# Kernel tuning notes

Hardware: AMD Instinct MI355X
Metric: run time of the kernel (lower is better)

The kernel has to match this reference:

```python
import jax, jax.numpy as jnp
import numpy as np

B, C, H, W = 8, 32, 256, 256


def setup_inputs() -> dict:
    key = jax.random.key(0)
    ks = jax.random.split(key, 9)
    x = jax.random.normal(ks[0], (B, C, H, W), dtype=jnp.float32)
    # depthwise 1x1 conv (groups=C) == per-channel scalar weight + bias
    def wb(kw, kb):
        w = jax.random.normal(kw, (C,), dtype=jnp.float32) * (1.0 / jnp.sqrt(1.0))
        b = jax.random.normal(kb, (C,), dtype=jnp.float32) * 0.1
        return w, b
    w_up, b_up = wb(ks[1], ks[2])
    w_right, b_right = wb(ks[3], ks[4])
    w_down, b_down = wb(ks[5], ks[6])
    w_left, b_left = wb(ks[7], ks[8])
    return {"x": x, "w_up": w_up, "b_up": b_up, "w_right": w_right,
            "b_right": b_right, "w_down": w_down, "b_down": b_down,
            "w_left": w_left, "b_left": b_left}


def _dir_scan(x_seq, w, b):
    """x_seq: [L, B, C, K]. h[0]=x[0]; h[t+1]=relu(w_c*h[t]+b_c+x[t+1])."""
    wb_ = w[None, :, None]
    bb_ = b[None, :, None]

    def step(h, xt):
        hn = jax.nn.relu(h * wb_ + bb_ + xt)
        return hn, hn

    _, ys = jax.lax.scan(step, x_seq[0], x_seq[1:])
    return jnp.concatenate([x_seq[:1], ys], axis=0)


def reference(x, w_up, b_up, w_right, b_right, w_down, b_down, w_left, b_left):
    xh = jnp.moveaxis(x, 2, 0)  # [H, B, C, W] for row scans
    xw = jnp.moveaxis(x, 3, 0)  # [W, B, C, H] for column scans

    top_down = jnp.moveaxis(_dir_scan(xh, w_down, b_down), 0, 2)
    top_up = jnp.moveaxis(_dir_scan(xh[::-1], w_up, b_up)[::-1], 0, 2)
    top_right = jnp.moveaxis(_dir_scan(xw, w_right, b_right), 0, 3)
    top_left = jnp.moveaxis(_dir_scan(xw[::-1], w_left, b_left)[::-1], 0, 3)

    return (top_up, top_right, top_down, top_left)
```

## Files before the change

### kernel.cpp

```cpp
#include <hip/hip_runtime.h>

#define BB 8
#define CC 32
#define HH 256
#define WW 256

#define CLAMP_BF16_MAX 3.3895313892515355e+38f

__device__ __forceinline__ float step_v6(float h, float w, float b, float x) {
    float t = __fadd_rn(__fadd_rn(__fmul_rn(h, w), b), x);
    float r;
    asm volatile(
        "v_max_f32 %0, %1, 0\n\t"
        "v_min_f32 %0, %0, %2"
        : "=&v"(r)
        : "v"(t), "v"(CLAMP_BF16_MAX));
    return r;
}

__global__ __launch_bounds__(256, 2) void scan_vert_v6(
    const float* __restrict__ x,
    const float* __restrict__ w_up,   const float* __restrict__ b_up,
    const float* __restrict__ w_down, const float* __restrict__ b_down,
    float* __restrict__ out_up, float* __restrict__ out_down)
{
    const int tid = blockIdx.x * 256 + threadIdx.x;
    const int w  = tid & (WW - 1);
    const int bc = tid >> 8;
    const int c  = bc & (CC - 1);
    const float* xp = x + (size_t)bc * (HH * WW) + w;

    if (blockIdx.y == 0) {
        const float wc = w_down[c], bb = b_down[c];
        float* op = out_down + (size_t)bc * (HH * WW) + w;
        float h = xp[0];
        op[0] = h;
        #pragma unroll 4
        for (int t = 1; t < HH; ++t) {
            float xv = xp[t * WW];
            h = step_v6(h, wc, bb, xv);
            op[t * WW] = h;
        }
    } else {
        const float wc = w_up[c], bb = b_up[c];
        float* op = out_up + (size_t)bc * (HH * WW) + w;
        float h = xp[(HH - 1) * WW];
        op[(HH - 1) * WW] = h;
        #pragma unroll 4
        for (int t = HH - 2; t >= 0; --t) {
            float xv = xp[t * WW];
            h = step_v6(h, wc, bb, xv);
            op[t * WW] = h;
        }
    }
}

__global__ __launch_bounds__(128, 2) void scan_horiz_v6(
    const float* __restrict__ x,
    const float* __restrict__ w_right, const float* __restrict__ b_right,
    const float* __restrict__ w_left,  const float* __restrict__ b_left,
    float* __restrict__ out_right, float* __restrict__ out_left)
{
    __shared__ __align__(16) float tile_v6[128 * 68];

    const int dir = blockIdx.y;
    const int tid = threadIdx.x;
    const long long R0 = (long long)blockIdx.x * 128;
    const int c = (int)((R0 >> 8) & (CC - 1));
    const float wc = dir ? w_left[c] : w_right[c];
    const float bb = dir ? b_left[c] : b_right[c];
    const float* xbase = x + R0 * WW;
    float* obase = (dir ? out_left : out_right) + R0 * WW;

    float h = 0.0f;
    for (int s = 0; s < 4; ++s) {
        const int tt = dir ? (3 - s) : s;
        const int w0 = tt * 64;

        #pragma unroll
        for (int it = 0; it < 16; ++it) {
            int idx = it * 128 + tid;
            int row = idx >> 4;
            int l   = idx & 15;
            float4 v = *(const float4*)(xbase + row * WW + w0 + l * 4);
            *(float4*)&tile_v6[row * 68 + l * 4] = v;
        }
        __syncthreads();

        float* trow = &tile_v6[tid * 68];
        if (dir == 0) {
            #pragma unroll
            for (int j = 0; j < 16; ++j) {
                float4 v = *(float4*)&trow[j * 4];
                if (s == 0 && j == 0) h = v.x;
                else h = step_v6(h, wc, bb, v.x);
                v.x = h;
                h = step_v6(h, wc, bb, v.y); v.y = h;
                h = step_v6(h, wc, bb, v.z); v.z = h;
                h = step_v6(h, wc, bb, v.w); v.w = h;
                *(float4*)&trow[j * 4] = v;
            }
        } else {
            #pragma unroll
            for (int j = 15; j >= 0; --j) {
                float4 v = *(float4*)&trow[j * 4];
                if (s == 0 && j == 15) h = v.w;
                else h = step_v6(h, wc, bb, v.w);
                v.w = h;
                h = step_v6(h, wc, bb, v.z); v.z = h;
                h = step_v6(h, wc, bb, v.y); v.y = h;
                h = step_v6(h, wc, bb, v.x); v.x = h;
                *(float4*)&trow[j * 4] = v;
            }
        }
        __syncthreads();

        #pragma unroll
        for (int it = 0; it < 16; ++it) {
            int idx = it * 128 + tid;
            int row = idx >> 4;
            int l   = idx & 15;
            float4 v = *(const float4*)&tile_v6[row * 68 + l * 4];
            *(float4*)(obase + row * WW + w0 + l * 4) = v;
        }
        __syncthreads();
    }
}

extern "C" void kernel_launch(void* const* d_in, const int* in_sizes, int n_in,
                              void* d_out, int out_size, void* d_ws, size_t ws_size,
                              hipStream_t stream) {
    const float* x       = (const float*)d_in[0];
    const float* w_up    = (const float*)d_in[1];
    const float* b_up    = (const float*)d_in[2];
    const float* w_right = (const float*)d_in[3];
    const float* b_right = (const float*)d_in[4];
    const float* w_down  = (const float*)d_in[5];
    const float* b_down  = (const float*)d_in[6];
    const float* w_left  = (const float*)d_in[7];
    const float* b_left  = (const float*)d_in[8];

    float* out = (float*)d_out;
    const long long N = (long long)BB * CC * HH * WW;
    float* out_up    = out;
    float* out_right = out + N;
    float* out_down  = out + 2 * N;
    float* out_left  = out + 3 * N;

    scan_vert_v6<<<dim3(BB * CC, 2), 256, 0, stream>>>(
        x, w_up, b_up, w_down, b_down, out_up, out_down);

    scan_horiz_v6<<<dim3((BB * CC * HH) / 128, 2), 128, 0, stream>>>(
        x, w_right, b_right, w_left, b_left, out_right, out_left);
}
```

Measured before the change: 413.5 us.

## Software-prefetch scan inputs in both kernels and use odd LDS row stride

The vertical scan kernel now keeps an 8-deep register buffer and prefetches the next 8 rows while computing the current ones, replacing the plain unroll-by-4 loop. The up and down directions are merged into one code path with a signed stride. The horizontal kernel pads LDS rows to 67 floats instead of 68 and switches to scalar LDS accesses to avoid bank conflicts in the per-thread row scan. It also prefetches 16-element chunks of each row into registers ahead of use. These changes aim to hide memory latency behind the serial dependency chain, at the cost of more registers and more LDS instructions.

```diff
diff --git a/kernel.cpp b/kernel.cpp
--- a/kernel.cpp
+++ b/kernel.cpp
@@ -5,20 +5,18 @@
 #define HH 256
 #define WW 256
 
-#define CLAMP_BF16_MAX 3.3895313892515355e+38f
-
-__device__ __forceinline__ float step_v6(float h, float w, float b, float x) {
+__device__ __forceinline__ float step_v7(float h, float w, float b, float x) {
     float t = __fadd_rn(__fadd_rn(__fmul_rn(h, w), b), x);
     float r;
     asm volatile(
         "v_max_f32 %0, %1, 0\n\t"
         "v_min_f32 %0, %0, %2"
         : "=&v"(r)
-        : "v"(t), "v"(CLAMP_BF16_MAX));
+        : "v"(t), "v"(3.3895313892515355e+38f));
     return r;
 }
 
-__global__ __launch_bounds__(256, 2) void scan_vert_v6(
+__global__ __launch_bounds__(256, 2) void scan_vert_v7(
     const float* __restrict__ x,
     const float* __restrict__ w_up,   const float* __restrict__ b_up,
     const float* __restrict__ w_down, const float* __restrict__ b_down,
@@ -28,47 +26,67 @@
     const int w  = tid & (WW - 1);
     const int bc = tid >> 8;
     const int c  = bc & (CC - 1);
-    const float* xp = x + (size_t)bc * (HH * WW) + w;
+    const bool down = (blockIdx.y == 0);
+    const float wc = down ? w_down[c] : w_up[c];
+    const float bv = down ? b_down[c] : b_up[c];
 
-    if (blockIdx.y == 0) {
-        const float wc = w_down[c], bb = b_down[c];
-        float* op = out_down + (size_t)bc * (HH * WW) + w;
-        float h = xp[0];
-        op[0] = h;
-        #pragma unroll 4
-        for (int t = 1; t < HH; ++t) {
-            float xv = xp[t * WW];
-            h = step_v6(h, wc, bb, xv);
-            op[t * WW] = h;
+    const long long base = (long long)bc * (HH * WW) + w;
+    const long long t0   = down ? 0 : (HH - 1);
+    const long long st   = down ? WW : -WW;
+    const float* xs = x + base + t0 * WW;
+    float*       os = (down ? out_down : out_up) + base + t0 * WW;
+
+    float h = xs[0];
+    os[0] = h;
+
+    float buf[8];
+    #pragma unroll
+    for (int i = 0; i < 8; ++i) buf[i] = xs[(1 + i) * st];
+
+    int kb = 1;
+    #pragma unroll 1
+    for (int g = 0; g < 30; ++g) {
+        float nb[8];
+        #pragma unroll
+        for (int i = 0; i < 8; ++i) nb[i] = xs[(kb + 8 + i) * st];
+        #pragma unroll
+        for (int i = 0; i < 8; ++i) {
+            h = step_v7(h, wc, bv, buf[i]);
+            os[(kb + i) * st] = h;
         }
-    } else {
-        const float wc = w_up[c], bb = b_up[c];
-        float* op = out_up + (size_t)bc * (HH * WW) + w;
-        float h = xp[(HH - 1) * WW];
-        op[(HH - 1) * WW] = h;
-        #pragma unroll 4
-        for (int t = HH - 2; t >= 0; --t) {
-            float xv = xp[t * WW];
-            h = step_v6(h, wc, bb, xv);
-            op[t * WW] = h;
-        }
+        #pragma unroll
+        for (int i = 0; i < 8; ++i) buf[i] = nb[i];
+        kb += 8;
+    }
+    float tb[7];
+    #pragma unroll
+    for (int i = 0; i < 7; ++i) tb[i] = xs[(249 + i) * st];
+    #pragma unroll
+    for (int i = 0; i < 8; ++i) {
+        h = step_v7(h, wc, bv, buf[i]);
+        os[(241 + i) * st] = h;
+    }
+    #pragma unroll
+    for (int i = 0; i < 7; ++i) {
+        h = step_v7(h, wc, bv, tb[i]);
+        os[(249 + i) * st] = h;
     }
 }
 
-__global__ __launch_bounds__(128, 2) void scan_horiz_v6(
+__global__ __launch_bounds__(128, 2) void scan_horiz_v7(
     const float* __restrict__ x,
     const float* __restrict__ w_right, const float* __restrict__ b_right,
     const float* __restrict__ w_left,  const float* __restrict__ b_left,
     float* __restrict__ out_right, float* __restrict__ out_left)
 {
-    __shared__ __align__(16) float tile_v6[128 * 68];
+    __shared__ float tile[128 * 67];
 
     const int dir = blockIdx.y;
     const int tid = threadIdx.x;
     const long long R0 = (long long)blockIdx.x * 128;
     const int c = (int)((R0 >> 8) & (CC - 1));
     const float wc = dir ? w_left[c] : w_right[c];
-    const float bb = dir ? b_left[c] : b_right[c];
+    const float bv = dir ? b_left[c] : b_right[c];
     const float* xbase = x + R0 * WW;
     float* obase = (dir ? out_left : out_right) + R0 * WW;
 
@@ -83,34 +101,58 @@
             int row = idx >> 4;
             int l   = idx & 15;
             float4 v = *(const float4*)(xbase + row * WW + w0 + l * 4);
-            *(float4*)&tile_v6[row * 68 + l * 4] = v;
+            int a = row * 67 + l * 4;
+            tile[a]     = v.x;
+            tile[a + 1] = v.y;
+            tile[a + 2] = v.z;
+            tile[a + 3] = v.w;
         }
         __syncthreads();
 
-        float* trow = &tile_v6[tid * 68];
+        float* trow = &tile[tid * 67];
         if (dir == 0) {
+            float rb[16];
             #pragma unroll
-            for (int j = 0; j < 16; ++j) {
-                float4 v = *(float4*)&trow[j * 4];
-                if (s == 0 && j == 0) h = v.x;
-                else h = step_v6(h, wc, bb, v.x);
-                v.x = h;
-                h = step_v6(h, wc, bb, v.y); v.y = h;
-                h = step_v6(h, wc, bb, v.z); v.z = h;
-                h = step_v6(h, wc, bb, v.w); v.w = h;
-                *(float4*)&trow[j * 4] = v;
+            for (int i = 0; i < 16; ++i) rb[i] = trow[i];
+            #pragma unroll
+            for (int q = 0; q < 4; ++q) {
+                float nb[16];
+                if (q < 3) {
+                    #pragma unroll
+                    for (int i = 0; i < 16; ++i) nb[i] = trow[16 * (q + 1) + i];
+                }
+                #pragma unroll
+                for (int i = 0; i < 16; ++i) {
+                    if (s == 0 && q == 0 && i == 0) h = rb[0];
+                    else h = step_v7(h, wc, bv, rb[i]);
+                    trow[16 * q + i] = h;
+                }
+                if (q < 3) {
+                    #pragma unroll
+                    for (int i = 0; i < 16; ++i) rb[i] = nb[i];
+                }
             }
         } else {
+            float rb[16];
             #pragma unroll
-            for (int j = 15; j >= 0; --j) {
-                float4 v = *(float4*)&trow[j * 4];
-                if (s == 0 && j == 15) h = v.w;
-                else h = step_v6(h, wc, bb, v.w);
-                v.w = h;
-                h = step_v6(h, wc, bb, v.z); v.z = h;
-                h = step_v6(h, wc, bb, v.y); v.y = h;
-                h = step_v6(h, wc, bb, v.x); v.x = h;
-                *(float4*)&trow[j * 4] = v;
+            for (int i = 0; i < 16; ++i) rb[i] = trow[48 + i];
+            #pragma unroll
+            for (int q = 3; q >= 0; --q) {
+                float nb[16];
+                if (q > 0) {
+                    #pragma unroll
+                    for (int i = 0; i < 16; ++i) nb[i] = trow[16 * (q - 1) + i];
+                }
+                #pragma unroll
+                for (int i = 15; i >= 0; --i) {
+                    if (s == 0 && q == 3 && i == 15) h = rb[15];
+                    else h = step_v7(h, wc, bv, rb[i]);
+                    trow[16 * q + i] = h;
+                }
+                if (q > 0) {
+                    #pragma unroll
+                    for (int i = 0; i < 16; ++i) rb[i] = nb[i];
+                }
             }
         }
         __syncthreads();
@@ -120,7 +162,8 @@
             int idx = it * 128 + tid;
             int row = idx >> 4;
             int l   = idx & 15;
-            float4 v = *(const float4*)&tile_v6[row * 68 + l * 4];
+            int a = row * 67 + l * 4;
+            float4 v = make_float4(tile[a], tile[a + 1], tile[a + 2], tile[a + 3]);
             *(float4*)(obase + row * WW + w0 + l * 4) = v;
         }
         __syncthreads();
@@ -147,9 +190,9 @@
     float* out_down  = out + 2 * N;
     float* out_left  = out + 3 * N;
 
-    scan_vert_v6<<<dim3(BB * CC, 2), 256, 0, stream>>>(
+    scan_vert_v7<<<dim3(BB * CC, 2), 256, 0, stream>>>(
         x, w_up, b_up, w_down, b_down, out_up, out_down);
 
-    scan_horiz_v6<<<dim3((BB * CC * HH) / 128, 2), 128, 0, stream>>>(
+    scan_horiz_v7<<<dim3((BB * CC * HH) / 128, 2), 128, 0, stream>>>(
         x, w_right, b_right, w_left, b_left, out_right, out_left);
 }
```

Measured after the change: 346.1 us. -16.3%, faster.
